# Optimization experiments

Hardware: AMD Instinct MI355X
Metric: run time of the kernel (lower is better)

The kernel has to match this reference:

```python
import math
import jax, jax.numpy as jnp
import numpy as np


def positionalencoding1d(d_model, length):
    # [length, d_model]; d_model must be even
    position = jnp.arange(length, dtype=jnp.float32)[:, None]
    div_term = jnp.exp(jnp.arange(0, d_model, 2, dtype=jnp.float32) * (-(math.log(10000.0) / d_model)))
    pe = jnp.zeros((length, d_model), dtype=jnp.float32)
    pe = pe.at[:, 0::2].set(jnp.sin(position * div_term))
    pe = pe.at[:, 1::2].set(jnp.cos(position * div_term))
    return pe


def setup_inputs() -> dict:
    key = jax.random.key(0)
    k1, k2, k3 = jax.random.split(key, 3)
    B, D, H, W = 64, 512, 32, 32
    NH = 8
    DH = D // NH
    x = jax.random.normal(k1, (B, D, H, W), dtype=jnp.float32)
    q = jax.random.normal(k2, (1, NH, 1, DH), dtype=jnp.float32)
    Wkv = jax.random.normal(k3, (D, 2 * D), dtype=jnp.float32) * 0.02
    bkv = jnp.zeros((2 * D,), dtype=jnp.float32)
    return {"x": x, "q": q, "Wkv": Wkv, "bkv": bkv, "num_heads": NH}


def reference(x, q, Wkv, bkv, num_heads):
    B, d, h, w = x.shape
    N = h * w
    NH = num_heads
    DH = d // NH
    scale = DH ** (-0.5)

    xt = x.reshape(B, d, N).transpose(0, 2, 1)            # b n d
    kv = xt @ Wkv + bkv                                   # b n 2d
    k, v = jnp.split(kv, 2, axis=-1)
    k = k.reshape(B, N, NH, DH).transpose(0, 2, 1, 3)     # b h n d
    v = v.reshape(B, N, NH, DH).transpose(0, 2, 1, 3)     # b h n d

    pe = positionalencoding1d(DH, N)                      # n d, broadcast over b,h
    k = k + pe

    qh = q[0, :, 0, :]                                    # h d (shared learned query)
    dots = jnp.einsum('hd,bhnd->bhn', qh, k) * scale      # b h n
    attn = jax.nn.softmax(dots, axis=-1)
    out = jnp.einsum('bhn,bhnd->bhd', attn, v)            # b h d
    return out.reshape(B, NH * DH)                        # b (h d)
```

## Files before the change

### kernel.cpp

```cpp
#include <hip/hip_runtime.h>
#include <math.h>

#define BATCH  64
#define DCH    512
#define NPOS   1024
#define NH     8
#define NSPLIT 16
#define NRANGE 64

__global__ __launch_bounds__(256) void k_prep(const float* __restrict__ q,
                                              const float* __restrict__ Wkv,
                                              const float* __restrict__ bkv,
                                              float* __restrict__ wqT,
                                              float* __restrict__ bias) {
    int blk = blockIdx.x;
    if (blk < 2) {
        int c = blk * 256 + threadIdx.x;
        const float4* wrow = (const float4*)(Wkv + (size_t)c * (2 * DCH));
        const float4* q4   = (const float4*)q;
        #pragma unroll
        for (int h = 0; h < NH; ++h) {
            float s = 0.f;
            #pragma unroll
            for (int d4 = 0; d4 < 16; ++d4) {
                float4 a = q4[h * 16 + d4];
                float4 w = wrow[h * 16 + d4];
                s = fmaf(a.x, w.x, fmaf(a.y, w.y, fmaf(a.z, w.z, fmaf(a.w, w.w, s))));
            }
            wqT[c * NH + h] = 0.125f * s;
        }
    } else {
        int n = (blk - 2) * 256 + threadIdx.x;
        float pq[NH];
        #pragma unroll
        for (int h = 0; h < NH; ++h) pq[h] = 0.f;
        const float kfac2 = -13.2877123795494f / 64.f;
        for (int i = 0; i < 32; ++i) {
            float dt = exp2f((float)(2 * i) * kfac2);
            float ang = (float)n * dt;
            float sn, cs;
            sincosf(ang, &sn, &cs);
            #pragma unroll
            for (int h = 0; h < NH; ++h)
                pq[h] = fmaf(q[h * 64 + 2 * i], sn,
                        fmaf(q[h * 64 + 2 * i + 1], cs, pq[h]));
        }
        #pragma unroll
        for (int h = 0; h < NH; ++h) {
            float bq = 0.f;
            #pragma unroll 8
            for (int d = 0; d < 64; ++d)
                bq = fmaf(q[h * 64 + d], bkv[h * 64 + d], bq);
            bias[h * NPOS + n] = 0.125f * (pq[h] + bq);
        }
    }
}

__global__ __launch_bounds__(512) void k_flash(const float* __restrict__ x,
                                               const float* __restrict__ wqT,
                                               const float* __restrict__ bias,
                                               float* __restrict__ apart,
                                               float* __restrict__ mz) {
    __shared__ float sred[8][NH][NRANGE];
    __shared__ float pbuf[NH][NRANGE];

    int b = blockIdx.y, ns = blockIdx.x;
    int t = threadIdx.x;
    int w = __builtin_amdgcn_readfirstlane(t >> 6);
    int lane = t & 63;
    int n0 = ns * NRANGE;
    int c0 = w * 64;

    {
        const float* xp = x + ((size_t)b * DCH + c0) * NPOS + n0 + lane;
        const float* wr = wqT + c0 * NH;
        float acc[NH];
        #pragma unroll
        for (int h = 0; h < NH; ++h) acc[h] = 0.f;

        float xv[8], xn[8];
        #pragma unroll
        for (int u = 0; u < 8; ++u) xv[u] = xp[(size_t)u * NPOS];

        #pragma unroll
        for (int g = 0; g < 8; ++g) {
            if (g < 7) {
                #pragma unroll
                for (int u = 0; u < 8; ++u)
                    xn[u] = xp[(size_t)(8 * g + 8 + u) * NPOS];
            }
            #pragma unroll
            for (int u = 0; u < 8; ++u) {
                float wv[8];
                *(float4*)&wv[0] = *(const float4*)(wr + (8 * g + u) * NH);
                *(float4*)&wv[4] = *(const float4*)(wr + (8 * g + u) * NH + 4);
                #pragma unroll
                for (int h = 0; h < NH; ++h)
                    acc[h] = fmaf(xv[u], wv[h], acc[h]);
            }
            if (g < 7) {
                #pragma unroll
                for (int u = 0; u < 8; ++u) xv[u] = xn[u];
            }
        }
        #pragma unroll
        for (int h = 0; h < NH; ++h) sred[w][h][lane] = acc[h];
    }
    __syncthreads();

    {
        float s = bias[w * NPOS + n0 + lane];
        #pragma unroll
        for (int o = 0; o < 8; ++o) s += sred[o][w][lane];
        float m = s;
        #pragma unroll
        for (int o = 32; o; o >>= 1) m = fmaxf(m, __shfl_xor(m, o));
        float p = expf(s - m);
        float z = p;
        #pragma unroll
        for (int o = 32; o; o >>= 1) z += __shfl_xor(z, o);
        pbuf[w][lane] = p;
        if (lane == 0) {
            float* mzp = mz + ((size_t)ns * BATCH + b) * 2 * NH;
            mzp[w]      = m;
            mzp[NH + w] = z;
        }
    }
    __syncthreads();

    {
        int rg = lane >> 2;
        int nq = lane & 3;
        const float* xr = x + ((size_t)b * DCH + c0 + rg) * NPOS + n0 + nq * 4;

        float con[4][NH];
        #pragma unroll
        for (int cp = 0; cp < 4; ++cp)
            #pragma unroll
            for (int h = 0; h < NH; ++h) con[cp][h] = 0.f;

        #pragma unroll
        for (int j = 0; j < 4; ++j) {
            float4 xv4[4];
            #pragma unroll
            for (int cp = 0; cp < 4; ++cp)
                xv4[cp] = *(const float4*)(xr + (size_t)(cp * 16) * NPOS + j * 16);
            float4 pj[NH];
            #pragma unroll
            for (int h = 0; h < NH; ++h)
                pj[h] = *(const float4*)&pbuf[h][j * 16 + nq * 4];
            #pragma unroll
            for (int cp = 0; cp < 4; ++cp)
                #pragma unroll
                for (int h = 0; h < NH; ++h)
                    con[cp][h] = fmaf(xv4[cp].x, pj[h].x, fmaf(xv4[cp].y, pj[h].y,
                                 fmaf(xv4[cp].z, pj[h].z, fmaf(xv4[cp].w, pj[h].w, con[cp][h]))));
        }

        #pragma unroll
        for (int cp = 0; cp < 4; ++cp)
            #pragma unroll
            for (int h = 0; h < NH; ++h) {
                float v = con[cp][h];
                v += __shfl_xor(v, 1);
                v += __shfl_xor(v, 2);
                con[cp][h] = v;
            }

        size_t abase = ((size_t)ns * BATCH + b) * (NH * DCH);
        #pragma unroll
        for (int cp = 0; cp < 4; ++cp) {
            int c = c0 + cp * 16 + rg;
            float lo = (nq == 0) ? con[cp][0] : (nq == 1) ? con[cp][1]
                     : (nq == 2) ? con[cp][2] : con[cp][3];
            float hi = (nq == 0) ? con[cp][4] : (nq == 1) ? con[cp][5]
                     : (nq == 2) ? con[cp][6] : con[cp][7];
            apart[abase + (size_t)nq * DCH + c]       = lo;
            apart[abase + (size_t)(nq + 4) * DCH + c] = hi;
        }
    }
}

__global__ __launch_bounds__(512) void k_comb(const float* __restrict__ apart,
                                              const float* __restrict__ mz,
                                              const float* __restrict__ Wkv,
                                              const float* __restrict__ bkv,
                                              float* __restrict__ out) {
    __shared__ float as[NH * DCH];
    __shared__ float red[2][256];
    int b = blockIdx.x, half = blockIdx.y, t = threadIdx.x;
    int h = t >> 6;

    float M = -1e30f;
    #pragma unroll
    for (int j = 0; j < NSPLIT; ++j)
        M = fmaxf(M, mz[((size_t)j * BATCH + b) * 2 * NH + h]);
    float Z = 0.f, fj[NSPLIT];
    #pragma unroll
    for (int j = 0; j < NSPLIT; ++j) {
        const float* mzp = mz + ((size_t)j * BATCH + b) * 2 * NH;
        fj[j] = expf(mzp[h] - M);
        Z = fmaf(fj[j], mzp[NH + h], Z);
    }
    float invZ = 1.f / Z;

    int e0 = t * 8;
    float v[8];
    #pragma unroll
    for (int k = 0; k < 8; ++k) v[k] = 0.f;
    #pragma unroll 4
    for (int j = 0; j < NSPLIT; ++j) {
        const float* src = apart + ((size_t)j * BATCH + b) * (NH * DCH) + e0;
        float4 lo = *(const float4*)(src);
        float4 hi = *(const float4*)(src + 4);
        v[0] = fmaf(fj[j], lo.x, v[0]);
        v[1] = fmaf(fj[j], lo.y, v[1]);
        v[2] = fmaf(fj[j], lo.z, v[2]);
        v[3] = fmaf(fj[j], lo.w, v[3]);
        v[4] = fmaf(fj[j], hi.x, v[4]);
        v[5] = fmaf(fj[j], hi.y, v[5]);
        v[6] = fmaf(fj[j], hi.z, v[6]);
        v[7] = fmaf(fj[j], hi.w, v[7]);
    }
    #pragma unroll
    for (int k = 0; k < 8; ++k) as[e0 + k] = v[k] * invZ;
    __syncthreads();

    int o  = t & 255;
    int cp = t >> 8;
    int hd = half * 256 + o;
    int ho = hd >> 6;
    float a0 = 0.f, a1 = 0.f, a2 = 0.f, a3 = 0.f;
    const float* wp  = Wkv + DCH + hd;
    const float* apr = as + ho * DCH;
    int cbeg = cp * 256;
    #pragma unroll 4
    for (int c = cbeg; c < cbeg + 256; c += 4) {
        a0 = fmaf(apr[c],     wp[(size_t)c * (2 * DCH)],       a0);
        a1 = fmaf(apr[c + 1], wp[(size_t)(c + 1) * (2 * DCH)], a1);
        a2 = fmaf(apr[c + 2], wp[(size_t)(c + 2) * (2 * DCH)], a2);
        a3 = fmaf(apr[c + 3], wp[(size_t)(c + 3) * (2 * DCH)], a3);
    }
    red[cp][o] = (a0 + a1) + (a2 + a3);
    __syncthreads();
    if (t < 256) {
        int hd2 = half * 256 + t;
        out[(size_t)b * DCH + hd2] = bkv[DCH + hd2] + red[0][t] + red[1][t];
    }
}

extern "C" void kernel_launch(void* const* d_in, const int* in_sizes, int n_in,
                              void* d_out, int out_size, void* d_ws, size_t ws_size,
                              hipStream_t stream) {
    const float* x   = (const float*)d_in[0];
    const float* q   = (const float*)d_in[1];
    const float* Wkv = (const float*)d_in[2];
    const float* bkv = (const float*)d_in[3];
    float* out = (float*)d_out;

    float* ws    = (float*)d_ws;
    float* wqT   = ws;
    float* bias  = wqT + DCH * NH;
    float* apart = bias + NH * NPOS;
    float* mz    = apart + (size_t)NSPLIT * BATCH * NH * DCH;

    hipLaunchKernelGGL(k_prep,  dim3(6),             dim3(256), 0, stream, q, Wkv, bkv, wqT, bias);
    hipLaunchKernelGGL(k_flash, dim3(NSPLIT, BATCH), dim3(512), 0, stream, x, wqT, bias, apart, mz);
    hipLaunchKernelGGL(k_comb,  dim3(BATCH, 2),      dim3(512), 0, stream, apart, mz, Wkv, bkv, out);
}
```

Measured before the change: 86.02 us.

## Stage query weights in LDS, vectorize score loads, prefetch x, use exp2

```diff
diff --git a/kernel.cpp b/kernel.cpp
--- a/kernel.cpp
+++ b/kernel.cpp
@@ -7,6 +7,7 @@
 #define NH     8
 #define NSPLIT 16
 #define NRANGE 64
+#define SCL    0.1803368801111244f
 
 __global__ __launch_bounds__(256) void k_prep(const float* __restrict__ q,
                                               const float* __restrict__ Wkv,
@@ -27,7 +28,7 @@
                 float4 w = wrow[h * 16 + d4];
                 s = fmaf(a.x, w.x, fmaf(a.y, w.y, fmaf(a.z, w.z, fmaf(a.w, w.w, s))));
             }
-            wqT[c * NH + h] = 0.125f * s;
+            wqT[c * NH + h] = SCL * s;
         }
     } else {
         int n = (blk - 2) * 256 + threadIdx.x;
@@ -51,61 +52,90 @@
             #pragma unroll 8
             for (int d = 0; d < 64; ++d)
                 bq = fmaf(q[h * 64 + d], bkv[h * 64 + d], bq);
-            bias[h * NPOS + n] = 0.125f * (pq[h] + bq);
-        }
-    }
-}
-
-__global__ __launch_bounds__(512) void k_flash(const float* __restrict__ x,
-                                               const float* __restrict__ wqT,
-                                               const float* __restrict__ bias,
-                                               float* __restrict__ apart,
-                                               float* __restrict__ mz) {
+            bias[h * NPOS + n] = SCL * (pq[h] + bq);
+        }
+    }
+}
+
+__global__ __launch_bounds__(512, 4) void k_flash(const float* __restrict__ x,
+                                                  const float* __restrict__ wqT,
+                                                  const float* __restrict__ bias,
+                                                  float* __restrict__ apart,
+                                                  float* __restrict__ mz) {
+    __shared__ float wqs[DCH * NH];
     __shared__ float sred[8][NH][NRANGE];
     __shared__ float pbuf[NH][NRANGE];
 
     int b = blockIdx.y, ns = blockIdx.x;
     int t = threadIdx.x;
-    int w = __builtin_amdgcn_readfirstlane(t >> 6);
+    int w = t >> 6;
     int lane = t & 63;
     int n0 = ns * NRANGE;
     int c0 = w * 64;
 
     {
-        const float* xp = x + ((size_t)b * DCH + c0) * NPOS + n0 + lane;
-        const float* wr = wqT + c0 * NH;
-        float acc[NH];
-        #pragma unroll
-        for (int h = 0; h < NH; ++h) acc[h] = 0.f;
-
-        float xv[8], xn[8];
-        #pragma unroll
-        for (int u = 0; u < 8; ++u) xv[u] = xp[(size_t)u * NPOS];
-
-        #pragma unroll
-        for (int g = 0; g < 8; ++g) {
-            if (g < 7) {
-                #pragma unroll
-                for (int u = 0; u < 8; ++u)
-                    xn[u] = xp[(size_t)(8 * g + 8 + u) * NPOS];
-            }
-            #pragma unroll
-            for (int u = 0; u < 8; ++u) {
-                float wv[8];
-                *(float4*)&wv[0] = *(const float4*)(wr + (8 * g + u) * NH);
-                *(float4*)&wv[4] = *(const float4*)(wr + (8 * g + u) * NH + 4);
-                #pragma unroll
-                for (int h = 0; h < NH; ++h)
-                    acc[h] = fmaf(xv[u], wv[h], acc[h]);
-            }
-            if (g < 7) {
-                #pragma unroll
-                for (int u = 0; u < 8; ++u) xv[u] = xn[u];
-            }
-        }
-        #pragma unroll
-        for (int h = 0; h < NH; ++h) sred[w][h][lane] = acc[h];
-    }
+        const float4* s = (const float4*)wqT;
+        float4* d = (float4*)wqs;
+        d[t] = s[t]; d[t + 512] = s[t + 512];
+    }
+    __syncthreads();
+
+    int rg = lane >> 4;
+    int n4 = lane & 15;
+    const float* gx = x + ((size_t)b * DCH + c0 + rg) * NPOS + n0 + n4 * 4;
+
+    float acc[NH][4];
+    #pragma unroll
+    for (int h = 0; h < NH; ++h)
+        #pragma unroll
+        for (int e = 0; e < 4; ++e) acc[h][e] = 0.f;
+
+    float4 xw[8];
+    #pragma unroll
+    for (int k = 0; k < 8; ++k)
+        xw[k] = *(const float4*)(gx + (size_t)(4 * k) * NPOS);
+
+    #pragma unroll
+    for (int k = 0; k < 16; ++k) {
+        float4 xv = xw[k & 7];
+        if (k < 8)
+            xw[k & 7] = *(const float4*)(gx + (size_t)(4 * (k + 8)) * NPOS);
+        int c = c0 + 4 * k + rg;
+        float wv[8];
+        *(float4*)&wv[0] = *(const float4*)&wqs[c * 8];
+        *(float4*)&wv[4] = *(const float4*)&wqs[c * 8 + 4];
+        #pragma unroll
+        for (int h = 0; h < NH; ++h) {
+            acc[h][0] = fmaf(xv.x, wv[h], acc[h][0]);
+            acc[h][1] = fmaf(xv.y, wv[h], acc[h][1]);
+            acc[h][2] = fmaf(xv.z, wv[h], acc[h][2]);
+            acc[h][3] = fmaf(xv.w, wv[h], acc[h][3]);
+        }
+    }
+    #pragma unroll
+    for (int h = 0; h < NH; ++h)
+        #pragma unroll
+        for (int e = 0; e < 4; ++e) {
+            float v = acc[h][e];
+            v += __shfl_xor(v, 16);
+            v += __shfl_xor(v, 32);
+            acc[h][e] = v;
+        }
+    if (rg == 0) {
+        #pragma unroll
+        for (int h = 0; h < NH; ++h)
+            *(float4*)&sred[w][h][n4 * 4] =
+                make_float4(acc[h][0], acc[h][1], acc[h][2], acc[h][3]);
+    }
+
+    int rg3 = lane >> 2;
+    int nq  = lane & 3;
+    const float* xr = x + ((size_t)b * DCH + c0 + rg3) * NPOS + n0 + nq * 4;
+    float4 xcur[4];
+    #pragma unroll
+    for (int cp = 0; cp < 4; ++cp)
+        xcur[cp] = *(const float4*)(xr + (size_t)(cp * 16) * NPOS);
+
     __syncthreads();
 
     {
@@ -115,7 +145,7 @@
         float m = s;
         #pragma unroll
         for (int o = 32; o; o >>= 1) m = fmaxf(m, __shfl_xor(m, o));
-        float p = expf(s - m);
+        float p = exp2f(s - m);
         float z = p;
         #pragma unroll
         for (int o = 32; o; o >>= 1) z += __shfl_xor(z, o);
@@ -129,10 +159,6 @@
     __syncthreads();
 
     {
-        int rg = lane >> 2;
-        int nq = lane & 3;
-        const float* xr = x + ((size_t)b * DCH + c0 + rg) * NPOS + n0 + nq * 4;
-
         float con[4][NH];
         #pragma unroll
         for (int cp = 0; cp < 4; ++cp)
@@ -141,10 +167,12 @@
 
         #pragma unroll
         for (int j = 0; j < 4; ++j) {
-            float4 xv4[4];
-            #pragma unroll
-            for (int cp = 0; cp < 4; ++cp)
-                xv4[cp] = *(const float4*)(xr + (size_t)(cp * 16) * NPOS + j * 16);
+            float4 xnx[4];
+            if (j < 3) {
+                #pragma unroll
+                for (int cp = 0; cp < 4; ++cp)
+                    xnx[cp] = *(const float4*)(xr + (size_t)(cp * 16) * NPOS + (j + 1) * 16);
+            }
             float4 pj[NH];
             #pragma unroll
             for (int h = 0; h < NH; ++h)
@@ -153,8 +181,12 @@
             for (int cp = 0; cp < 4; ++cp)
                 #pragma unroll
                 for (int h = 0; h < NH; ++h)
-                    con[cp][h] = fmaf(xv4[cp].x, pj[h].x, fmaf(xv4[cp].y, pj[h].y,
-                                 fmaf(xv4[cp].z, pj[h].z, fmaf(xv4[cp].w, pj[h].w, con[cp][h]))));
+                    con[cp][h] = fmaf(xcur[cp].x, pj[h].x, fmaf(xcur[cp].y, pj[h].y,
+                                 fmaf(xcur[cp].z, pj[h].z, fmaf(xcur[cp].w, pj[h].w, con[cp][h]))));
+            if (j < 3) {
+                #pragma unroll
+                for (int cp = 0; cp < 4; ++cp) xcur[cp] = xnx[cp];
+            }
         }
 
         #pragma unroll
@@ -170,7 +202,7 @@
         size_t abase = ((size_t)ns * BATCH + b) * (NH * DCH);
         #pragma unroll
         for (int cp = 0; cp < 4; ++cp) {
-            int c = c0 + cp * 16 + rg;
+            int c = c0 + cp * 16 + rg3;
             float lo = (nq == 0) ? con[cp][0] : (nq == 1) ? con[cp][1]
                      : (nq == 2) ? con[cp][2] : con[cp][3];
             float hi = (nq == 0) ? con[cp][4] : (nq == 1) ? con[cp][5]
@@ -186,10 +218,12 @@
                                               const float* __restrict__ Wkv,
                                               const float* __restrict__ bkv,
                                               float* __restrict__ out) {
-    __shared__ float as[NH * DCH];
+    __shared__ float as[2048];
     __shared__ float red[2][256];
     int b = blockIdx.x, half = blockIdx.y, t = threadIdx.x;
-    int h = t >> 6;
+
+    int e0 = t * 4;
+    int h  = half * 4 + (t >> 7);
 
     float M = -1e30f;
     #pragma unroll
@@ -199,40 +233,34 @@
     #pragma unroll
     for (int j = 0; j < NSPLIT; ++j) {
         const float* mzp = mz + ((size_t)j * BATCH + b) * 2 * NH;
-        fj[j] = expf(mzp[h] - M);
+        fj[j] = exp2f(mzp[h] - M);
         Z = fmaf(fj[j], mzp[NH + h], Z);
     }
     float invZ = 1.f / Z;
 
-    int e0 = t * 8;
-    float v[8];
-    #pragma unroll
-    for (int k = 0; k < 8; ++k) v[k] = 0.f;
+    float v0 = 0.f, v1 = 0.f, v2 = 0.f, v3 = 0.f;
     #pragma unroll 4
     for (int j = 0; j < NSPLIT; ++j) {
-        const float* src = apart + ((size_t)j * BATCH + b) * (NH * DCH) + e0;
-        float4 lo = *(const float4*)(src);
-        float4 hi = *(const float4*)(src + 4);
-        v[0] = fmaf(fj[j], lo.x, v[0]);
-        v[1] = fmaf(fj[j], lo.y, v[1]);
-        v[2] = fmaf(fj[j], lo.z, v[2]);
-        v[3] = fmaf(fj[j], lo.w, v[3]);
-        v[4] = fmaf(fj[j], hi.x, v[4]);
-        v[5] = fmaf(fj[j], hi.y, v[5]);
-        v[6] = fmaf(fj[j], hi.z, v[6]);
-        v[7] = fmaf(fj[j], hi.w, v[7]);
-    }
-    #pragma unroll
-    for (int k = 0; k < 8; ++k) as[e0 + k] = v[k] * invZ;
+        const float* src = apart + ((size_t)j * BATCH + b) * (NH * DCH)
+                         + half * 2048 + e0;
+        float4 lo = *(const float4*)src;
+        v0 = fmaf(fj[j], lo.x, v0);
+        v1 = fmaf(fj[j], lo.y, v1);
+        v2 = fmaf(fj[j], lo.z, v2);
+        v3 = fmaf(fj[j], lo.w, v3);
+    }
+    as[e0]     = v0 * invZ;
+    as[e0 + 1] = v1 * invZ;
+    as[e0 + 2] = v2 * invZ;
+    as[e0 + 3] = v3 * invZ;
     __syncthreads();
 
     int o  = t & 255;
     int cp = t >> 8;
     int hd = half * 256 + o;
-    int ho = hd >> 6;
     float a0 = 0.f, a1 = 0.f, a2 = 0.f, a3 = 0.f;
     const float* wp  = Wkv + DCH + hd;
-    const float* apr = as + ho * DCH;
+    const float* apr = as + (o >> 6) * DCH;
     int cbeg = cp * 256;
     #pragma unroll 4
     for (int c = cbeg; c < cbeg + 256; c += 4) {
```

After: 88.65 us. 3.1% more time.

## Split fused flash kernel into dots, softmax, and PV passes

Applied to the files above, without the earlier changes.

```diff
diff --git a/kernel.cpp b/kernel.cpp
--- a/kernel.cpp
+++ b/kernel.cpp
@@ -5,8 +5,8 @@
 #define DCH    512
 #define NPOS   1024
 #define NH     8
-#define NSPLIT 16
-#define NRANGE 64
+#define NSPLIT 8
+#define SCL    0.1803368801111244f
 
 __global__ __launch_bounds__(256) void k_prep(const float* __restrict__ q,
                                               const float* __restrict__ Wkv,
@@ -27,7 +27,7 @@
                 float4 w = wrow[h * 16 + d4];
                 s = fmaf(a.x, w.x, fmaf(a.y, w.y, fmaf(a.z, w.z, fmaf(a.w, w.w, s))));
             }
-            wqT[c * NH + h] = 0.125f * s;
+            wqT[c * NH + h] = SCL * s;
         }
     } else {
         int n = (blk - 2) * 256 + threadIdx.x;
@@ -51,188 +51,173 @@
             #pragma unroll 8
             for (int d = 0; d < 64; ++d)
                 bq = fmaf(q[h * 64 + d], bkv[h * 64 + d], bq);
-            bias[h * NPOS + n] = 0.125f * (pq[h] + bq);
-        }
-    }
-}
-
-__global__ __launch_bounds__(512) void k_flash(const float* __restrict__ x,
-                                               const float* __restrict__ wqT,
-                                               const float* __restrict__ bias,
-                                               float* __restrict__ apart,
-                                               float* __restrict__ mz) {
-    __shared__ float sred[8][NH][NRANGE];
-    __shared__ float pbuf[NH][NRANGE];
-
+            bias[h * NPOS + n] = SCL * (pq[h] + bq);
+        }
+    }
+}
+
+__global__ __launch_bounds__(512) void k_dots(const float* __restrict__ x,
+                                              const float* __restrict__ wqT,
+                                              const float* __restrict__ bias,
+                                              float* __restrict__ dots) {
+    __shared__ float sred[8][NH][64];
+    int b = blockIdx.y, nt = blockIdx.x;
+    int t = threadIdx.x, w = t >> 6, lane = t & 63;
+    int n0 = nt * 64, c0 = w * 64;
+
+    float bv = bias[w * NPOS + n0 + lane];
+
+    const float* xp = x + ((size_t)b * DCH + c0) * NPOS + n0 + lane;
+    const float* wr = wqT + c0 * NH;
+
+    float acc[NH];
+    #pragma unroll
+    for (int h = 0; h < NH; ++h) acc[h] = 0.f;
+
+    float xw[8];
+    #pragma unroll
+    for (int u = 0; u < 8; ++u) xw[u] = xp[(size_t)u * NPOS];
+
+    #pragma unroll
+    for (int k = 0; k < 64; ++k) {
+        float xv = xw[k & 7];
+        if (k < 56)
+            xw[k & 7] = xp[(size_t)(k + 8) * NPOS];
+        float wv[8];
+        *(float4*)&wv[0] = *(const float4*)(wr + k * 8);
+        *(float4*)&wv[4] = *(const float4*)(wr + k * 8 + 4);
+        #pragma unroll
+        for (int h = 0; h < NH; ++h)
+            acc[h] = fmaf(xv, wv[h], acc[h]);
+    }
+    #pragma unroll
+    for (int h = 0; h < NH; ++h) sred[w][h][lane] = acc[h];
+    __syncthreads();
+
+    float s = bv;
+    #pragma unroll
+    for (int o = 0; o < 8; ++o) s += sred[o][w][lane];
+    dots[((size_t)b * NH + w) * NPOS + n0 + lane] = s;
+}
+
+__global__ __launch_bounds__(512) void k_soft(const float* __restrict__ dots,
+                                              float* __restrict__ attn) {
+    int b = blockIdx.x, t = threadIdx.x, w = t >> 6, lane = t & 63;
+    const float* p = dots + ((size_t)b * NH + w) * NPOS;
+    float v[16], m = -1e30f;
+    #pragma unroll
+    for (int j = 0; j < 16; ++j) {
+        v[j] = p[lane + 64 * j];
+        m = fmaxf(m, v[j]);
+    }
+    #pragma unroll
+    for (int o = 32; o; o >>= 1) m = fmaxf(m, __shfl_xor(m, o));
+    float z = 0.f;
+    #pragma unroll
+    for (int j = 0; j < 16; ++j) { v[j] = exp2f(v[j] - m); z += v[j]; }
+    #pragma unroll
+    for (int o = 32; o; o >>= 1) z += __shfl_xor(z, o);
+    float inv = 1.f / z;
+    float* q = attn + ((size_t)b * NH + w) * NPOS;
+    #pragma unroll
+    for (int j = 0; j < 16; ++j) q[lane + 64 * j] = v[j] * inv;
+}
+
+__global__ __launch_bounds__(512, 4) void k_pv(const float* __restrict__ x,
+                                               const float* __restrict__ attn,
+                                               float* __restrict__ apart) {
+    __shared__ float pls[NH][128];
     int b = blockIdx.y, ns = blockIdx.x;
-    int t = threadIdx.x;
-    int w = __builtin_amdgcn_readfirstlane(t >> 6);
-    int lane = t & 63;
-    int n0 = ns * NRANGE;
+    int t = threadIdx.x, w = t >> 6, lane = t & 63;
+    int n0 = ns * 128;
+
+    if (t < 256) {
+        int h = t >> 5, i = t & 31;
+        ((float4*)&pls[h][0])[i] =
+            ((const float4*)(attn + ((size_t)b * NH + h) * NPOS + n0))[i];
+    }
+    __syncthreads();
+
+    int rg = lane >> 2, nq = lane & 3;
     int c0 = w * 64;
-
-    {
-        const float* xp = x + ((size_t)b * DCH + c0) * NPOS + n0 + lane;
-        const float* wr = wqT + c0 * NH;
-        float acc[NH];
-        #pragma unroll
-        for (int h = 0; h < NH; ++h) acc[h] = 0.f;
-
-        float xv[8], xn[8];
-        #pragma unroll
-        for (int u = 0; u < 8; ++u) xv[u] = xp[(size_t)u * NPOS];
-
-        #pragma unroll
-        for (int g = 0; g < 8; ++g) {
-            if (g < 7) {
-                #pragma unroll
-                for (int u = 0; u < 8; ++u)
-                    xn[u] = xp[(size_t)(8 * g + 8 + u) * NPOS];
-            }
-            #pragma unroll
-            for (int u = 0; u < 8; ++u) {
-                float wv[8];
-                *(float4*)&wv[0] = *(const float4*)(wr + (8 * g + u) * NH);
-                *(float4*)&wv[4] = *(const float4*)(wr + (8 * g + u) * NH + 4);
-                #pragma unroll
-                for (int h = 0; h < NH; ++h)
-                    acc[h] = fmaf(xv[u], wv[h], acc[h]);
-            }
-            if (g < 7) {
-                #pragma unroll
-                for (int u = 0; u < 8; ++u) xv[u] = xn[u];
-            }
-        }
-        #pragma unroll
-        for (int h = 0; h < NH; ++h) sred[w][h][lane] = acc[h];
-    }
-    __syncthreads();
-
-    {
-        float s = bias[w * NPOS + n0 + lane];
-        #pragma unroll
-        for (int o = 0; o < 8; ++o) s += sred[o][w][lane];
-        float m = s;
-        #pragma unroll
-        for (int o = 32; o; o >>= 1) m = fmaxf(m, __shfl_xor(m, o));
-        float p = expf(s - m);
-        float z = p;
-        #pragma unroll
-        for (int o = 32; o; o >>= 1) z += __shfl_xor(z, o);
-        pbuf[w][lane] = p;
-        if (lane == 0) {
-            float* mzp = mz + ((size_t)ns * BATCH + b) * 2 * NH;
-            mzp[w]      = m;
-            mzp[NH + w] = z;
-        }
-    }
-    __syncthreads();
-
-    {
-        int rg = lane >> 2;
-        int nq = lane & 3;
-        const float* xr = x + ((size_t)b * DCH + c0 + rg) * NPOS + n0 + nq * 4;
-
-        float con[4][NH];
+    const float* xr = x + ((size_t)b * DCH + c0 + rg) * NPOS + n0 + nq * 4;
+
+    float con[4][NH];
+    #pragma unroll
+    for (int cp = 0; cp < 4; ++cp)
+        #pragma unroll
+        for (int h = 0; h < NH; ++h) con[cp][h] = 0.f;
+
+    #pragma unroll
+    for (int j = 0; j < 8; ++j) {
+        float4 xv[4];
+        #pragma unroll
+        for (int cp = 0; cp < 4; ++cp)
+            xv[cp] = *(const float4*)(xr + (size_t)(cp * 16) * NPOS + j * 16);
+        float4 pj[NH];
+        #pragma unroll
+        for (int h = 0; h < NH; ++h)
+            pj[h] = *(const float4*)&pls[h][j * 16 + nq * 4];
         #pragma unroll
         for (int cp = 0; cp < 4; ++cp)
             #pragma unroll
-            for (int h = 0; h < NH; ++h) con[cp][h] = 0.f;
-
-        #pragma unroll
-        for (int j = 0; j < 4; ++j) {
-            float4 xv4[4];
-            #pragma unroll
-            for (int cp = 0; cp < 4; ++cp)
-                xv4[cp] = *(const float4*)(xr + (size_t)(cp * 16) * NPOS + j * 16);
-            float4 pj[NH];
-            #pragma unroll
             for (int h = 0; h < NH; ++h)
-                pj[h] = *(const float4*)&pbuf[h][j * 16 + nq * 4];
-            #pragma unroll
-            for (int cp = 0; cp < 4; ++cp)
-                #pragma unroll
-                for (int h = 0; h < NH; ++h)
-                    con[cp][h] = fmaf(xv4[cp].x, pj[h].x, fmaf(xv4[cp].y, pj[h].y,
-                                 fmaf(xv4[cp].z, pj[h].z, fmaf(xv4[cp].w, pj[h].w, con[cp][h]))));
-        }
-
-        #pragma unroll
-        for (int cp = 0; cp < 4; ++cp)
-            #pragma unroll
-            for (int h = 0; h < NH; ++h) {
-                float v = con[cp][h];
-                v += __shfl_xor(v, 1);
-                v += __shfl_xor(v, 2);
-                con[cp][h] = v;
-            }
-
-        size_t abase = ((size_t)ns * BATCH + b) * (NH * DCH);
-        #pragma unroll
-        for (int cp = 0; cp < 4; ++cp) {
-            int c = c0 + cp * 16 + rg;
-            float lo = (nq == 0) ? con[cp][0] : (nq == 1) ? con[cp][1]
-                     : (nq == 2) ? con[cp][2] : con[cp][3];
-            float hi = (nq == 0) ? con[cp][4] : (nq == 1) ? con[cp][5]
-                     : (nq == 2) ? con[cp][6] : con[cp][7];
-            apart[abase + (size_t)nq * DCH + c]       = lo;
-            apart[abase + (size_t)(nq + 4) * DCH + c] = hi;
-        }
+                con[cp][h] = fmaf(xv[cp].x, pj[h].x, fmaf(xv[cp].y, pj[h].y,
+                             fmaf(xv[cp].z, pj[h].z, fmaf(xv[cp].w, pj[h].w, con[cp][h]))));
+    }
+
+    #pragma unroll
+    for (int cp = 0; cp < 4; ++cp)
+        #pragma unroll
+        for (int h = 0; h < NH; ++h) {
+            float v = con[cp][h];
+            v += __shfl_xor(v, 1);
+            v += __shfl_xor(v, 2);
+            con[cp][h] = v;
+        }
+
+    size_t abase = ((size_t)ns * BATCH + b) * (NH * DCH);
+    #pragma unroll
+    for (int cp = 0; cp < 4; ++cp) {
+        int c = c0 + cp * 16 + rg;
+        float lo = (nq == 0) ? con[cp][0] : (nq == 1) ? con[cp][1]
+                 : (nq == 2) ? con[cp][2] : con[cp][3];
+        float hi = (nq == 0) ? con[cp][4] : (nq == 1) ? con[cp][5]
+                 : (nq == 2) ? con[cp][6] : con[cp][7];
+        apart[abase + (size_t)nq * DCH + c]       = lo;
+        apart[abase + (size_t)(nq + 4) * DCH + c] = hi;
     }
 }
 
 __global__ __launch_bounds__(512) void k_comb(const float* __restrict__ apart,
-                                              const float* __restrict__ mz,
                                               const float* __restrict__ Wkv,
                                               const float* __restrict__ bkv,
                                               float* __restrict__ out) {
-    __shared__ float as[NH * DCH];
+    __shared__ float as[2048];
     __shared__ float red[2][256];
     int b = blockIdx.x, half = blockIdx.y, t = threadIdx.x;
-    int h = t >> 6;
-
-    float M = -1e30f;
-    #pragma unroll
-    for (int j = 0; j < NSPLIT; ++j)
-        M = fmaxf(M, mz[((size_t)j * BATCH + b) * 2 * NH + h]);
-    float Z = 0.f, fj[NSPLIT];
+
+    int e0 = t * 4;
+    float v0 = 0.f, v1 = 0.f, v2 = 0.f, v3 = 0.f;
     #pragma unroll
     for (int j = 0; j < NSPLIT; ++j) {
-        const float* mzp = mz + ((size_t)j * BATCH + b) * 2 * NH;
-        fj[j] = expf(mzp[h] - M);
-        Z = fmaf(fj[j], mzp[NH + h], Z);
-    }
-    float invZ = 1.f / Z;
-
-    int e0 = t * 8;
-    float v[8];
-    #pragma unroll
-    for (int k = 0; k < 8; ++k) v[k] = 0.f;
-    #pragma unroll 4
-    for (int j = 0; j < NSPLIT; ++j) {
-        const float* src = apart + ((size_t)j * BATCH + b) * (NH * DCH) + e0;
-        float4 lo = *(const float4*)(src);
-        float4 hi = *(const float4*)(src + 4);
-        v[0] = fmaf(fj[j], lo.x, v[0]);
-        v[1] = fmaf(fj[j], lo.y, v[1]);
-        v[2] = fmaf(fj[j], lo.z, v[2]);
-        v[3] = fmaf(fj[j], lo.w, v[3]);
-        v[4] = fmaf(fj[j], hi.x, v[4]);
-        v[5] = fmaf(fj[j], hi.y, v[5]);
-        v[6] = fmaf(fj[j], hi.z, v[6]);
-        v[7] = fmaf(fj[j], hi.w, v[7]);
-    }
-    #pragma unroll
-    for (int k = 0; k < 8; ++k) as[e0 + k] = v[k] * invZ;
+        const float* src = apart + ((size_t)j * BATCH + b) * (NH * DCH)
+                         + half * 2048 + e0;
+        float4 lo = *(const float4*)src;
+        v0 += lo.x; v1 += lo.y; v2 += lo.z; v3 += lo.w;
+    }
+    as[e0]     = v0;
+    as[e0 + 1] = v1;
+    as[e0 + 2] = v2;
+    as[e0 + 3] = v3;
     __syncthreads();
 
     int o  = t & 255;
     int cp = t >> 8;
     int hd = half * 256 + o;
-    int ho = hd >> 6;
     float a0 = 0.f, a1 = 0.f, a2 = 0.f, a3 = 0.f;
     const float* wp  = Wkv + DCH + hd;
-    const float* apr = as + ho * DCH;
+    const float* apr = as + (o >> 6) * DCH;
     int cbeg = cp * 256;
     #pragma unroll 4
     for (int c = cbeg; c < cbeg + 256; c += 4) {
@@ -261,10 +246,13 @@
     float* ws    = (float*)d_ws;
     float* wqT   = ws;
     float* bias  = wqT + DCH * NH;
-    float* apart = bias + NH * NPOS;
-    float* mz    = apart + (size_t)NSPLIT * BATCH * NH * DCH;
-
-    hipLaunchKernelGGL(k_prep,  dim3(6),             dim3(256), 0, stream, q, Wkv, bkv, wqT, bias);
-    hipLaunchKernelGGL(k_flash, dim3(NSPLIT, BATCH), dim3(512), 0, stream, x, wqT, bias, apart, mz);
-    hipLaunchKernelGGL(k_comb,  dim3(BATCH, 2),      dim3(512), 0, stream, apart, mz, Wkv, bkv, out);
-}
+    float* dots  = bias + NH * NPOS;
+    float* attn  = dots + (size_t)BATCH * NH * NPOS;
+    float* apart = attn + (size_t)BATCH * NH * NPOS;
+
+    hipLaunchKernelGGL(k_prep, dim3(6),             dim3(256), 0, stream, q, Wkv, bkv, wqT, bias);
+    hipLaunchKernelGGL(k_dots, dim3(16, BATCH),     dim3(512), 0, stream, x, wqT, bias, dots);
+    hipLaunchKernelGGL(k_soft, dim3(BATCH),         dim3(512), 0, stream, dots, attn);
+    hipLaunchKernelGGL(k_pv,   dim3(NSPLIT, BATCH), dim3(512), 0, stream, x, attn, apart);
+    hipLaunchKernelGGL(k_comb, dim3(BATCH, 2),      dim3(512), 0, stream, apart, Wkv, bkv, out);
+}
```

Result: slower. 116.7 us (+35.6%).
